# Kernel optimization log

Measured on AMD Instinct MI355X. Metric: run time of the kernel, lower is better.

## Reference

```python
import jax, jax.numpy as jnp
import numpy as np

HEADS = 12
WINDOW = 128

def setup_inputs() -> dict:
    key = jax.random.key(0)
    ks = jax.random.split(key, 5)
    B, N, C = 1, 4096, 768
    return {
        'x': jax.random.normal(ks[0], (B, N, C), dtype=jnp.float32),
        'qkv_w': jax.random.normal(ks[1], (3 * C, C), dtype=jnp.float32) * 0.02,
        'qkv_b': jax.random.normal(ks[2], (3 * C,), dtype=jnp.float32) * 0.02,
        'proj_w': jax.random.normal(ks[3], (C, C), dtype=jnp.float32) * 0.02,
        'proj_b': jax.random.normal(ks[4], (C,), dtype=jnp.float32) * 0.02,
    }

def reference(x, qkv_w, qkv_b, proj_w, proj_b):
    B, N, C = x.shape
    H = HEADS
    hd = C // H
    # qkv projection (torch Linear: y = x @ W^T + b)
    qkv = x @ qkv_w.T + qkv_b                      # [B, N, 3C]
    qkv = qkv.reshape(B, N, 3, H, hd).transpose(2, 0, 3, 1, 4)  # [3, B, H, N, hd]
    q, k, v = qkv[0], qkv[1], qkv[2]               # each [B, H, N, hd]
    # local (banded) mask: |i - j| <= window_size
    idxs = jnp.arange(N)
    local = jnp.abs(idxs[:, None] - idxs[None, :]) <= WINDOW  # [N, N] bool
    # dense scores then mask (faithful to original O(N^2) math)
    attn = jnp.einsum('bhnd,bhmd->bhnm', q, k) / jnp.sqrt(jnp.float32(hd))
    attn = jnp.where(local[None, None], attn, -jnp.inf)
    attn = jax.nn.softmax(attn, axis=-1)
    out = jnp.einsum('bhnm,bhmd->bhnd', attn, v)   # [B, H, N, hd]
    out = out.transpose(0, 2, 1, 3).reshape(B, N, C)
    return out @ proj_w.T + proj_b
```

## Files before the change

kernel.cpp:

```cpp
#include <hip/hip_runtime.h>
#include <hip/hip_fp16.h>
#include <cmath>

typedef _Float16 f16;
typedef __attribute__((ext_vector_type(8))) _Float16 f16x8;
typedef __attribute__((ext_vector_type(4))) _Float16 f16x4;
typedef __attribute__((ext_vector_type(4))) float f32x4;

#define EXP2F(x) __builtin_amdgcn_exp2f(x)

__global__ void cast3_f32_f16(const float* __restrict__ s0, f16* __restrict__ d0, int n0,
                              const float* __restrict__ s1, f16* __restrict__ d1, int n1,
                              const float* __restrict__ s2, f16* __restrict__ d2, int n2) {
    int i = blockIdx.x * blockDim.x + threadIdx.x;
    const float* s; f16* d; int j;
    if (i < n0)                { s = s0; d = d0; j = i; }
    else if (i < n0 + n1)      { s = s1; d = d1; j = i - n0; }
    else if (i < n0 + n1 + n2) { s = s2; d = d2; j = i - n0 - n1; }
    else return;
    float4 v = ((const float4*)s)[j];
    f16x4 o = { (f16)v.x, (f16)v.y, (f16)v.z, (f16)v.w };
    ((f16x4*)d)[j] = o;
}

__device__ __forceinline__ void store4(f16* p, const f32x4& v) {
    f16x4 o = { (f16)v[0], (f16)v[1], (f16)v[2], (f16)v[3] };
    *(f16x4*)p = o;
}
__device__ __forceinline__ void store4(float* p, const f32x4& v) {
    float4 o = { v[0], v[1], v[2], v[3] };
    *(float4*)p = o;
}

template <int WR, int WC, int MT, int NT, typename OT>
__global__ __launch_bounds__(256) void gemm_f16_pipe(
    const f16* __restrict__ A,
    const f16* __restrict__ W,
    const float* __restrict__ bias,
    OT* __restrict__ out,
    int M, int N, int K)
{
    constexpr int ACH = WR * MT;
    constexpr int BCH = WC * NT;
    constexpr int AR  = ACH / 4;
    constexpr int BR  = BCH / 4;
    __shared__ f16 Ash[2][ACH * 512];
    __shared__ f16 Bsh[2][BCH * 512];

    const int tid  = threadIdx.x;
    const int lane = tid & 63;
    const int w    = tid >> 6;
    const int wr   = w / WC;
    const int wc   = w % WC;
    const int lr   = lane & 15;
    const int lq   = lane >> 4;
    const int bm   = blockIdx.y * (WR * MT * 16);
    const int bn   = blockIdx.x * (WC * NT * 16);

    const f16* ga[AR];
    const f16* gb[BR];
#pragma unroll
    for (int r = 0; r < AR; ++r)
        ga[r] = A + (size_t)(bm + (w * AR + r) * 16 + lr) * K + lq * 8;
#pragma unroll
    for (int r = 0; r < BR; ++r)
        gb[r] = W + (size_t)(bn + (w * BR + r) * 16 + lr) * K + lq * 8;

    f32x4 acc[MT][NT] = {};
    f16x8 sa[AR], sb[BR];

#pragma unroll
    for (int r = 0; r < AR; ++r) sa[r] = *(const f16x8*)(ga[r]);
#pragma unroll
    for (int r = 0; r < BR; ++r) sb[r] = *(const f16x8*)(gb[r]);
#pragma unroll
    for (int r = 0; r < AR; ++r) *(f16x8*)&Ash[0][(w * AR + r) * 512 + lane * 8] = sa[r];
#pragma unroll
    for (int r = 0; r < BR; ++r) *(f16x8*)&Bsh[0][(w * BR + r) * 512 + lane * 8] = sb[r];
    __syncthreads();

    const int nk = K >> 5;
    for (int k = 0; k < nk; ++k) {
        const int cur = k & 1;
        if (k + 1 < nk) {
            const int ko = (k + 1) << 5;
#pragma unroll
            for (int r = 0; r < AR; ++r) sa[r] = *(const f16x8*)(ga[r] + ko);
#pragma unroll
            for (int r = 0; r < BR; ++r) sb[r] = *(const f16x8*)(gb[r] + ko);
        }
        f16x8 af[MT], bf[NT];
#pragma unroll
        for (int mt = 0; mt < MT; ++mt)
            af[mt] = *(const f16x8*)&Ash[cur][(wr * MT + mt) * 512 + lane * 8];
#pragma unroll
        for (int nt = 0; nt < NT; ++nt)
            bf[nt] = *(const f16x8*)&Bsh[cur][(wc * NT + nt) * 512 + lane * 8];
#pragma unroll
        for (int mt = 0; mt < MT; ++mt)
#pragma unroll
            for (int nt = 0; nt < NT; ++nt)
                acc[mt][nt] = __builtin_amdgcn_mfma_f32_16x16x32_f16(
                    bf[nt], af[mt], acc[mt][nt], 0, 0, 0);
        if (k + 1 < nk) {
#pragma unroll
            for (int r = 0; r < AR; ++r)
                *(f16x8*)&Ash[cur ^ 1][(w * AR + r) * 512 + lane * 8] = sa[r];
#pragma unroll
            for (int r = 0; r < BR; ++r)
                *(f16x8*)&Bsh[cur ^ 1][(w * BR + r) * 512 + lane * 8] = sb[r];
        }
        __syncthreads();
    }

#pragma unroll
    for (int mt = 0; mt < MT; ++mt) {
        int row = bm + (wr * MT + mt) * 16 + lr;
#pragma unroll
        for (int nt = 0; nt < NT; ++nt) {
            int col = bn + (wc * NT + nt) * 16 + lq * 4;
            float4 bv = *(const float4*)(bias + col);
            f32x4 ov = acc[mt][nt];
            ov[0] += bv.x; ov[1] += bv.y; ov[2] += bv.z; ov[3] += bv.w;
            store4(out + (size_t)row * N + col, ov);
        }
    }
}

#define WINDOW_SZ 128

__global__ __launch_bounds__(256) void local_attn_mfma(
    const f16* __restrict__ qkv,
    f16* __restrict__ out,
    int N)
{
    const int C  = 768;
    const int C3 = 2304;
    __shared__ f16 Ks[2][4096];
    __shared__ f16 Vt[2][4096];
    __shared__ f16 Ps[4096];

    const int tid  = threadIdx.x;
    const int lane = tid & 63;
    const int w    = tid >> 6;
    const int r15  = lane & 15;
    const int q4   = lane >> 4;
    const int ntiles = N >> 6;
    const int h  = blockIdx.x / ntiles;
    const int i0 = (blockIdx.x % ntiles) << 6;
    const int qoff = h * 64;
    const int koff = 768 + h * 64;
    const int voff = 1536 + h * 64;

    f16x8 qf[2];
    {
        const f16* qrow = qkv + (size_t)(i0 + w * 16 + r15) * C3 + qoff + q4 * 8;
        qf[0] = *(const f16x8*)(qrow);
        qf[1] = *(const f16x8*)(qrow + 32);
        const f16 qs = (f16)0.18033688f;
#pragma unroll
        for (int j = 0; j < 8; ++j) { qf[0][j] *= qs; qf[1][j] *= qs; }
    }

    const int vc0 = tid >> 3;
    const int vd0 = (tid & 7) * 8;
    const int va  = vd0 >> 3;

    f32x4 o[4] = {};
    float m_l = -1.0e30f, l_l = 0.f;

    const int lo = (i0 >= 128) ? 0 : ((128 - i0) >> 6);
    int hi = (N + 64 - i0) >> 6; if (hi > 4) hi = 4;

    f16x8 k0, k1, v0, v1;
    {
        int jbase = i0 - 128 + lo * 64;
        const f16* kr = qkv + (size_t)(jbase + w * 16 + r15) * C3 + koff + q4 * 8;
        k0 = *(const f16x8*)(kr);
        k1 = *(const f16x8*)(kr + 32);
        v0 = *(const f16x8*)(qkv + (size_t)(jbase + vc0) * C3 + voff + vd0);
        v1 = *(const f16x8*)(qkv + (size_t)(jbase + vc0 + 32) * C3 + voff + vd0);
        *(f16x8*)&Ks[0][(w * 2 + 0) * 512 + lane * 8] = k0;
        *(f16x8*)&Ks[0][(w * 2 + 1) * 512 + lane * 8] = k1;
        int cc0 = vc0 >> 3, c7 = vc0 & 7;
#pragma unroll
        for (int j = 0; j < 8; ++j) {
            Vt[0][(vd0 + j) * 64 + ((cc0 ^ va ^ j) & 7) * 8 + c7] = v0[j];
            Vt[0][(vd0 + j) * 64 + (((cc0 + 4) ^ va ^ j) & 7) * 8 + c7] = v1[j];
        }
    }
    __syncthreads();

    for (int ch = lo; ch <= hi; ++ch) {
        const int p = (ch - lo) & 1;
        const int jbase = i0 - 128 + ch * 64;
        const bool need_mask = (ch == 0) || (ch == 4);

        if (ch < hi) {
            int jn = jbase + 64;
            const f16* kr = qkv + (size_t)(jn + w * 16 + r15) * C3 + koff + q4 * 8;
            k0 = *(const f16x8*)(kr);
            k1 = *(const f16x8*)(kr + 32);
            v0 = *(const f16x8*)(qkv + (size_t)(jn + vc0) * C3 + voff + vd0);
            v1 = *(const f16x8*)(qkv + (size_t)(jn + vc0 + 32) * C3 + voff + vd0);
        }

        f32x4 s[4] = {};
#pragma unroll
        for (int ks = 0; ks < 2; ++ks)
#pragma unroll
            for (int nt = 0; nt < 4; ++nt) {
                f16x8 kf = *(const f16x8*)&Ks[p][(nt * 2 + ks) * 512 + lane * 8];
                s[nt] = __builtin_amdgcn_mfma_f32_16x16x32_f16(kf, qf[ks], s[nt], 0, 0, 0);
            }

        if (need_mask) {
            int qg = i0 + w * 16 + r15;
#pragma unroll
            for (int nt = 0; nt < 4; ++nt)
#pragma unroll
                for (int r = 0; r < 4; ++r) {
                    int dist = qg - (jbase + nt * 16 + q4 * 4 + r);
                    if (dist < 0) dist = -dist;
                    if (dist > WINDOW_SZ) s[nt][r] = -3.0e38f;
                }
        }

        float rmax = -3.0e38f;
#pragma unroll
        for (int nt = 0; nt < 4; ++nt)
#pragma unroll
            for (int r = 0; r < 4; ++r) rmax = fmaxf(rmax, s[nt][r]);
        rmax = fmaxf(rmax, __shfl_xor(rmax, 16));
        rmax = fmaxf(rmax, __shfl_xor(rmax, 32));
        float mn = fmaxf(m_l, rmax);
        float al = EXP2F(m_l - mn);
        m_l = mn;
        float rs = 0.f;
#pragma unroll
        for (int nt = 0; nt < 4; ++nt)
#pragma unroll
            for (int r = 0; r < 4; ++r) {
                float pv = EXP2F(s[nt][r] - mn);
                s[nt][r] = pv;
                rs += pv;
            }
        rs += __shfl_xor(rs, 16);
        rs += __shfl_xor(rs, 32);
        l_l = l_l * al + rs;
#pragma unroll
        for (int nd = 0; nd < 4; ++nd)
#pragma unroll
            for (int r = 0; r < 4; ++r) o[nd][r] *= al;

#pragma unroll
        for (int nt = 0; nt < 4; ++nt)
#pragma unroll
            for (int r = 0; r < 4; ++r) {
                int c  = nt * 16 + q4 * 4 + r;
                int cs = c >> 5;
                int c5 = c & 31;
                int ls = (c5 >> 3) * 16 + r15;
                int lss = ls ^ ((ls >> 3) & 7);
                Ps[(w * 2 + cs) * 512 + lss * 8 + (c5 & 7)] = (f16)s[nt][r];
            }

        int lssr = lane ^ ((lane >> 3) & 7);
#pragma unroll
        for (int cs = 0; cs < 2; ++cs) {
            f16x8 pf = *(const f16x8*)&Ps[(w * 2 + cs) * 512 + lssr * 8];
#pragma unroll
            for (int nd = 0; nd < 4; ++nd) {
                int d = nd * 16 + r15;
                int x = ((cs * 4 + q4) ^ (d >> 3) ^ d) & 7;
                f16x8 vf = *(const f16x8*)&Vt[p][d * 64 + x * 8];
                o[nd] = __builtin_amdgcn_mfma_f32_16x16x32_f16(vf, pf, o[nd], 0, 0, 0);
            }
        }

        if (ch < hi) {
            *(f16x8*)&Ks[p ^ 1][(w * 2 + 0) * 512 + lane * 8] = k0;
            *(f16x8*)&Ks[p ^ 1][(w * 2 + 1) * 512 + lane * 8] = k1;
            int cc0 = vc0 >> 3, c7 = vc0 & 7;
#pragma unroll
            for (int j = 0; j < 8; ++j) {
                Vt[p ^ 1][(vd0 + j) * 64 + ((cc0 ^ va ^ j) & 7) * 8 + c7] = v0[j];
                Vt[p ^ 1][(vd0 + j) * 64 + (((cc0 + 4) ^ va ^ j) & 7) * 8 + c7] = v1[j];
            }
        }
        __syncthreads();
    }

    float inv = 1.0f / l_l;
    int row = i0 + w * 16 + r15;
#pragma unroll
    for (int nd = 0; nd < 4; ++nd) {
        f16x4 ov = { (f16)(o[nd][0] * inv), (f16)(o[nd][1] * inv),
                     (f16)(o[nd][2] * inv), (f16)(o[nd][3] * inv) };
        *(f16x4*)(out + (size_t)row * C + qoff + nd * 16 + q4 * 4) = ov;
    }
}

extern "C" void kernel_launch(void* const* d_in, const int* in_sizes, int n_in,
                              void* d_out, int out_size, void* d_ws, size_t ws_size,
                              hipStream_t stream) {
    (void)n_in; (void)out_size; (void)ws_size;
    const float* x      = (const float*)d_in[0];
    const float* qkv_w  = (const float*)d_in[1];
    const float* qkv_b  = (const float*)d_in[2];
    const float* proj_w = (const float*)d_in[3];
    const float* proj_b = (const float*)d_in[4];
    float* outp = (float*)d_out;

    const int C    = in_sizes[2] / 3;
    const int Nseq = in_sizes[0] / C;
    const int C3   = 3 * C;

    char* ws = (char*)d_ws;
    f16* qkv_h = (f16*)ws;   ws += (size_t)Nseq * C3 * 2;
    f16* xh    = (f16*)ws;   ws += (size_t)Nseq * C * 2;
    f16* wh_q  = (f16*)ws;   ws += (size_t)C3 * C * 2;
    f16* wh_p  = (f16*)ws;
    f16* attn_h = xh;

    dim3 blk(256);
    {
        int n0 = Nseq * C / 4, n1 = C3 * C / 4, n2 = C * C / 4;
        int tot = n0 + n1 + n2;
        cast3_f32_f16<<<dim3((tot + 255) / 256), blk, 0, stream>>>(
            x, xh, n0, qkv_w, wh_q, n1, proj_w, wh_p, n2);
    }
    gemm_f16_pipe<2, 2, 4, 4, f16><<<dim3(C3 / 128, Nseq / 128), blk, 0, stream>>>(
        xh, wh_q, qkv_b, qkv_h, Nseq, C3, C);
    local_attn_mfma<<<dim3((C / 64) * (Nseq / 64)), blk, 0, stream>>>(
        qkv_h, attn_h, Nseq);
    gemm_f16_pipe<2, 2, 2, 2, float><<<dim3(C / 64, Nseq / 64), blk, 0, stream>>>(
        attn_h, wh_p, proj_b, outp, Nseq, C, C);
}
```

Before: 159.8 us.

## Pre-pack GEMM operands into MFMA fragment layout and double K step per stage

The cast kernel now writes x and both weight matrices as contiguous 16x32 fragment chunks (512 halves each) instead of row-major, and the attention kernel writes its output in the same packed layout. The GEMMs then load fully contiguous 1 KB chunks per wave and process 64 K per pipeline stage, which halves the number of barriers and gives more MFMAs per sync. This targets strided global loads and sync overhead, at the cost of more shared memory per block and scattered small stores in the attention epilogue.

```diff
diff --git a/kernel.cpp b/kernel.cpp
--- a/kernel.cpp
+++ b/kernel.cpp
@@ -9,18 +9,27 @@
 
 #define EXP2F(x) __builtin_amdgcn_exp2f(x)
 
-__global__ void cast3_f32_f16(const float* __restrict__ s0, f16* __restrict__ d0, int n0,
-                              const float* __restrict__ s1, f16* __restrict__ d1, int n1,
-                              const float* __restrict__ s2, f16* __restrict__ d2, int n2) {
-    int i = blockIdx.x * blockDim.x + threadIdx.x;
-    const float* s; f16* d; int j;
-    if (i < n0)                { s = s0; d = d0; j = i; }
-    else if (i < n0 + n1)      { s = s1; d = d1; j = i - n0; }
-    else if (i < n0 + n1 + n2) { s = s2; d = d2; j = i - n0 - n1; }
+
+__global__ void pack3_f32_f16(
+    const float* __restrict__ s0, f16* __restrict__ d0, int nc0, int kc0,
+    const float* __restrict__ s1, f16* __restrict__ d1, int nc1, int kc1,
+    const float* __restrict__ s2, f16* __restrict__ d2, int nc2, int kc2)
+{
+    int wid  = (blockIdx.x * blockDim.x + threadIdx.x) >> 6;
+    int lane = threadIdx.x & 63;
+    const float* s; f16* d; int cid, KC;
+    if (wid < nc0)                  { s = s0; d = d0; cid = wid;             KC = kc0; }
+    else if (wid < nc0 + nc1)       { s = s1; d = d1; cid = wid - nc0;       KC = kc1; }
+    else if (wid < nc0 + nc1 + nc2) { s = s2; d = d2; cid = wid - nc0 - nc1; KC = kc2; }
     else return;
-    float4 v = ((const float4*)s)[j];
-    f16x4 o = { (f16)v.x, (f16)v.y, (f16)v.z, (f16)v.w };
-    ((f16x4*)d)[j] = o;
+    int rc = cid / KC, kc = cid % KC;
+    int K  = KC << 5;
+    const float* src = s + (size_t)(rc * 16 + (lane & 15)) * K + kc * 32 + (lane >> 4) * 8;
+    float4 v0 = *(const float4*)src;
+    float4 v1 = *(const float4*)(src + 4);
+    f16x8 o = { (f16)v0.x, (f16)v0.y, (f16)v0.z, (f16)v0.w,
+                (f16)v1.x, (f16)v1.y, (f16)v1.z, (f16)v1.w };
+    *(f16x8*)(d + (size_t)cid * 512 + lane * 8) = o;
 }
 
 __device__ __forceinline__ void store4(f16* p, const f32x4& v) {
@@ -33,15 +42,16 @@
 }
 
 template <int WR, int WC, int MT, int NT, typename OT>
-__global__ __launch_bounds__(256) void gemm_f16_pipe(
-    const f16* __restrict__ A,
-    const f16* __restrict__ W,
+__global__ __launch_bounds__(256) void gemm_f16_packed(
+    const f16* __restrict__ Ap,
+    const f16* __restrict__ Wp,
     const float* __restrict__ bias,
     OT* __restrict__ out,
     int M, int N, int K)
 {
-    constexpr int ACH = WR * MT;
-    constexpr int BCH = WC * NT;
+    constexpr int KK  = 2;
+    constexpr int ACH = WR * MT * KK;
+    constexpr int BCH = WC * NT * KK;
     constexpr int AR  = ACH / 4;
     constexpr int BR  = BCH / 4;
     __shared__ f16 Ash[2][ACH * 512];
@@ -56,15 +66,20 @@
     const int lq   = lane >> 4;
     const int bm   = blockIdx.y * (WR * MT * 16);
     const int bn   = blockIdx.x * (WC * NT * 16);
+    const int KC   = K >> 5;
 
     const f16* ga[AR];
     const f16* gb[BR];
 #pragma unroll
-    for (int r = 0; r < AR; ++r)
-        ga[r] = A + (size_t)(bm + (w * AR + r) * 16 + lr) * K + lq * 8;
-#pragma unroll
-    for (int r = 0; r < BR; ++r)
-        gb[r] = W + (size_t)(bn + (w * BR + r) * 16 + lr) * K + lq * 8;
+    for (int r = 0; r < AR; ++r) {
+        int s = w * AR + r, rl = s / KK, kk = s % KK;
+        ga[r] = Ap + ((size_t)((bm >> 4) + rl) * KC + kk) * 512 + lane * 8;
+    }
+#pragma unroll
+    for (int r = 0; r < BR; ++r) {
+        int s = w * BR + r, rl = s / KK, kk = s % KK;
+        gb[r] = Wp + ((size_t)((bn >> 4) + rl) * KC + kk) * 512 + lane * 8;
+    }
 
     f32x4 acc[MT][NT] = {};
     f16x8 sa[AR], sb[BR];
@@ -79,29 +94,35 @@
     for (int r = 0; r < BR; ++r) *(f16x8*)&Bsh[0][(w * BR + r) * 512 + lane * 8] = sb[r];
     __syncthreads();
 
-    const int nk = K >> 5;
+    const int nk = K >> 6;
     for (int k = 0; k < nk; ++k) {
         const int cur = k & 1;
         if (k + 1 < nk) {
-            const int ko = (k + 1) << 5;
+            const int ko = (k + 1) * KK * 512;
 #pragma unroll
             for (int r = 0; r < AR; ++r) sa[r] = *(const f16x8*)(ga[r] + ko);
 #pragma unroll
             for (int r = 0; r < BR; ++r) sb[r] = *(const f16x8*)(gb[r] + ko);
         }
-        f16x8 af[MT], bf[NT];
+        f16x8 af[MT][KK], bf[NT][KK];
 #pragma unroll
         for (int mt = 0; mt < MT; ++mt)
-            af[mt] = *(const f16x8*)&Ash[cur][(wr * MT + mt) * 512 + lane * 8];
+#pragma unroll
+            for (int kk = 0; kk < KK; ++kk)
+                af[mt][kk] = *(const f16x8*)&Ash[cur][((wr * MT + mt) * KK + kk) * 512 + lane * 8];
 #pragma unroll
         for (int nt = 0; nt < NT; ++nt)
-            bf[nt] = *(const f16x8*)&Bsh[cur][(wc * NT + nt) * 512 + lane * 8];
-#pragma unroll
-        for (int mt = 0; mt < MT; ++mt)
-#pragma unroll
-            for (int nt = 0; nt < NT; ++nt)
-                acc[mt][nt] = __builtin_amdgcn_mfma_f32_16x16x32_f16(
-                    bf[nt], af[mt], acc[mt][nt], 0, 0, 0);
+#pragma unroll
+            for (int kk = 0; kk < KK; ++kk)
+                bf[nt][kk] = *(const f16x8*)&Bsh[cur][((wc * NT + nt) * KK + kk) * 512 + lane * 8];
+#pragma unroll
+        for (int kk = 0; kk < KK; ++kk)
+#pragma unroll
+            for (int mt = 0; mt < MT; ++mt)
+#pragma unroll
+                for (int nt = 0; nt < NT; ++nt)
+                    acc[mt][nt] = __builtin_amdgcn_mfma_f32_16x16x32_f16(
+                        bf[nt][kk], af[mt][kk], acc[mt][nt], 0, 0, 0);
         if (k + 1 < nk) {
 #pragma unroll
             for (int r = 0; r < AR; ++r)
@@ -131,7 +152,7 @@
 
 __global__ __launch_bounds__(256) void local_attn_mfma(
     const f16* __restrict__ qkv,
-    f16* __restrict__ out,
+    f16* __restrict__ outp,
     int N)
 {
     const int C  = 768;
@@ -292,12 +313,16 @@
     }
 
     float inv = 1.0f / l_l;
-    int row = i0 + w * 16 + r15;
+    const int KC2 = C >> 5;
+    const int rc  = (i0 >> 4) + w;
 #pragma unroll
     for (int nd = 0; nd < 4; ++nd) {
+        int col = qoff + nd * 16 + q4 * 4;
+        int kc  = col >> 5;
+        int lp  = r15 + ((col >> 3) & 3) * 16;
         f16x4 ov = { (f16)(o[nd][0] * inv), (f16)(o[nd][1] * inv),
                      (f16)(o[nd][2] * inv), (f16)(o[nd][3] * inv) };
-        *(f16x4*)(out + (size_t)row * C + qoff + nd * 16 + q4 * 4) = ov;
+        *(f16x4*)(outp + ((size_t)rc * KC2 + kc) * 512 + lp * 8 + (col & 7)) = ov;
     }
 }
 
@@ -315,25 +340,28 @@
     const int C    = in_sizes[2] / 3;
     const int Nseq = in_sizes[0] / C;
     const int C3   = 3 * C;
+    const int KC   = C >> 5;
 
     char* ws = (char*)d_ws;
     f16* qkv_h = (f16*)ws;   ws += (size_t)Nseq * C3 * 2;
-    f16* xh    = (f16*)ws;   ws += (size_t)Nseq * C * 2;
-    f16* wh_q  = (f16*)ws;   ws += (size_t)C3 * C * 2;
-    f16* wh_p  = (f16*)ws;
-    f16* attn_h = xh;
+    f16* xp    = (f16*)ws;   ws += (size_t)Nseq * C * 2;
+    f16* wqp   = (f16*)ws;   ws += (size_t)C3 * C * 2;
+    f16* wpp   = (f16*)ws;
+    f16* attn_p = xp;
 
     dim3 blk(256);
     {
-        int n0 = Nseq * C / 4, n1 = C3 * C / 4, n2 = C * C / 4;
-        int tot = n0 + n1 + n2;
-        cast3_f32_f16<<<dim3((tot + 255) / 256), blk, 0, stream>>>(
-            x, xh, n0, qkv_w, wh_q, n1, proj_w, wh_p, n2);
-    }
-    gemm_f16_pipe<2, 2, 4, 4, f16><<<dim3(C3 / 128, Nseq / 128), blk, 0, stream>>>(
-        xh, wh_q, qkv_b, qkv_h, Nseq, C3, C);
+        int nc0 = (Nseq / 16) * KC;
+        int nc1 = (C3 / 16) * KC;
+        int nc2 = (C / 16) * KC;
+        int nwaves = nc0 + nc1 + nc2;
+        pack3_f32_f16<<<dim3((nwaves + 3) / 4), blk, 0, stream>>>(
+            x, xp, nc0, KC, qkv_w, wqp, nc1, KC, proj_w, wpp, nc2, KC);
+    }
+    gemm_f16_packed<2, 2, 4, 4, f16><<<dim3(C3 / 128, Nseq / 128), blk, 0, stream>>>(
+        xp, wqp, qkv_b, qkv_h, Nseq, C3, C);
     local_attn_mfma<<<dim3((C / 64) * (Nseq / 64)), blk, 0, stream>>>(
-        qkv_h, attn_h, Nseq);
-    gemm_f16_pipe<2, 2, 2, 2, float><<<dim3(C / 64, Nseq / 64), blk, 0, stream>>>(
-        attn_h, wh_p, proj_b, outp, Nseq, C, C);
-}
+        qkv_h, attn_p, Nseq);
+    gemm_f16_packed<2, 2, 2, 2, float><<<dim3(C / 64, Nseq / 64), blk, 0, stream>>>(
+        attn_p, wpp, proj_b, outp, Nseq, C, C);
+}
```

After: 133.3 us. 1.2x faster.
